# Performance work log

Measured on AMD Instinct MI355X. Metric: run time of the kernel, lower is better.

The kernel has to match this reference:

```python
import jax, jax.numpy as jnp
import numpy as np

B, T, D, H, C = 256, 512, 128, 512, 10

def setup_inputs() -> dict:
    key = jax.random.key(0)
    ks = jax.random.split(key, 16)
    def kn(k, shape):  # kaiming-normal-ish init (gain irrelevant for correctness)
        fan_in = shape[-1]
        return jax.random.normal(k, shape, dtype=jnp.float32) * (1.0 / np.sqrt(fan_in))
    return {
        "x": jax.random.randint(ks[0], (B, T), 0, 3),
        "emb": jax.random.normal(ks[1], (3, D), dtype=jnp.float32),
        "Wfx": kn(ks[2], (H, D)), "Wfh": kn(ks[3], (H, H)), "bf": jnp.zeros((H,), jnp.float32),
        "Wix": kn(ks[4], (H, D)), "Wih": kn(ks[5], (H, H)), "bi": jnp.zeros((H,), jnp.float32),
        "Wox": kn(ks[6], (H, D)), "Woh": kn(ks[7], (H, H)), "bo": jnp.zeros((H,), jnp.float32),
        "Wcx": kn(ks[8], (H, D)), "bc": jnp.zeros((H,), jnp.float32),
        "Wph": kn(ks[9], (C, H)), "bp": jnp.zeros((C,), jnp.float32),
    }

def _forward(x, emb, Wfx, Wfh, bf, Wix, Wih, bi, Wox, Woh, bo, Wcx, bc, Wph, bp):
    xe = emb[x]  # [B, T, D]
    # Precompute input-to-gate projections as one big batched matmul each.
    fx = jnp.einsum('btd,hd->bth', xe, Wfx) + bf  # [B, T, H]
    ix = jnp.einsum('btd,hd->bth', xe, Wix) + bi
    ox = jnp.einsum('btd,hd->bth', xe, Wox) + bo
    cx = jnp.einsum('btd,hd->bth', xe, Wcx) + bc
    gates = jnp.stack([fx, ix, ox, cx], axis=0).transpose(2, 1, 0, 3)  # [T, B, 4, H]

    def step(carry, g):
        c, _ = carry
        gf, gi, go, gc = g[:, 0], g[:, 1], g[:, 2], g[:, 3]  # each [B, H]
        f = jax.nn.sigmoid(gf + c @ Wfh.T)
        i = jax.nn.sigmoid(gi + c @ Wih.T)
        o = jax.nn.sigmoid(go + c @ Woh.T)
        c_new = jax.nn.sigmoid(gc) * i + c * f
        h = jnp.tanh(c_new) * o
        return (c_new, h), None

    c0 = jnp.zeros((x.shape[0], Wfh.shape[0]), jnp.float32)
    (c_fin, h_fin), _ = jax.lax.scan(step, (c0, c0), gates)
    p = h_fin @ Wph.T + bp
    return jax.nn.log_softmax(p, axis=1)

def reference(x, emb, Wfx, Wfh, bf, Wix, Wih, bi, Wox, Woh, bo, Wcx, bc, Wph, bp):
    return _forward(x, emb, Wfx, Wfh, bf, Wix, Wih, bi, Wox, Woh, bo, Wcx, bc, Wph, bp)
```

## Files before the change

### kernel.cpp

```cpp
#include <hip/hip_runtime.h>
#include <stdint.h>

#define TLEN 512
#define HDIM 512
#define DDIM 128
#define NCLS 10

typedef float f32x4 __attribute__((ext_vector_type(4)));
typedef short bf16x8 __attribute__((ext_vector_type(8)));

__device__ __forceinline__ unsigned short f2bf(float f) {
  union { float f; unsigned u; } v; v.f = f;
  return (unsigned short)((v.u + 0x7FFFu + ((v.u >> 16) & 1u)) >> 16);
}
__device__ __forceinline__ float bf2f(unsigned short h) {
  union { unsigned u; float f; } v; v.u = ((unsigned)h) << 16; return v.f;
}
__device__ __forceinline__ float sigm(float x) {
  return __builtin_amdgcn_rcpf(1.0f + __expf(-x));
}
__device__ __forceinline__ void ast16(unsigned short* p, unsigned short v) {
  __hip_atomic_store(p, v, __ATOMIC_RELAXED, __HIP_MEMORY_SCOPE_AGENT);
}
__device__ __forceinline__ void astd(unsigned* p, unsigned v) {
  __hip_atomic_store(p, v, __ATOMIC_RELAXED, __HIP_MEMORY_SCOPE_AGENT);
}

#define GLOAD_SC1(dst, addr) \
  asm volatile("global_load_dwordx4 %0, %1, off sc1" : "=&v"(dst) : "v"(addr))
#define VMWAIT() do { asm volatile("s_waitcnt vmcnt(0)" ::: "memory"); \
                      __builtin_amdgcn_sched_barrier(0); } while (0)

__global__ void k_gates(const float* __restrict__ emb,
                        const float* __restrict__ Wfx, const float* __restrict__ bf_,
                        const float* __restrict__ Wix, const float* __restrict__ bi_,
                        const float* __restrict__ Wcx, const float* __restrict__ bc_,
                        const float* __restrict__ Wox, const float* __restrict__ bo_,
                        float* __restrict__ G) {
  int tid = blockIdx.x * 256 + threadIdx.x;
  int h = tid & (HDIM - 1);
  int v = (tid >> 9) % 3;
  int g = tid / (3 * HDIM);
  const float* W; const float* bb;
  if (g == 0)      { W = Wfx; bb = bf_; }
  else if (g == 1) { W = Wix; bb = bi_; }
  else if (g == 2) { W = Wcx; bb = bc_; }
  else             { W = Wox; bb = bo_; }
  const float* e = emb + v * DDIM;
  const float* w = W + h * DDIM;
  float s = bb[h];
  #pragma unroll 8
  for (int d = 0; d < DDIM; ++d) s += e[d] * w[d];
  if (g == 2) s = sigm(s);
  G[tid] = s;
}

__global__ void k_pack_fi(const float* __restrict__ Wfh, const float* __restrict__ Wih,
                          unsigned short* __restrict__ pk) {
  int tid = blockIdx.x * 256 + threadIdx.x;
  int l  = tid & 63;
  int kt = (tid >> 6) & 15;
  int g  = (tid >> 10) & 1;
  int nt = (tid >> 11) & 3;
  int hs = (tid >> 13) & 7;
  int n  = hs * 64 + nt * 16 + (l & 15);
  int k0 = kt * 32 + (l >> 4) * 8;
  const float* src = (g ? Wih : Wfh) + n * HDIM + k0;
  unsigned short* dst = pk + (size_t)tid * 8;
  #pragma unroll
  for (int e = 0; e < 8; ++e) dst[e] = f2bf(src[e]);
}

__global__ void k_pack_o(const float* __restrict__ Woh, unsigned short* __restrict__ pk) {
  int tid = blockIdx.x * 256 + threadIdx.x;
  int l  = tid & 63;
  int kt = (tid >> 6) & 15;
  int nt = (tid >> 10) & 3;
  int hs = (tid >> 12) & 7;
  int n  = hs * 64 + nt * 16 + (l & 15);
  int k0 = kt * 32 + (l >> 4) * 8;
  const float* src = Woh + n * HDIM + k0;
  unsigned short* dst = pk + (size_t)tid * 8;
  #pragma unroll
  for (int e = 0; e < 8; ++e) dst[e] = f2bf(src[e]);
}

__global__ __launch_bounds__(256, 1)
void k_scan(const int* __restrict__ x, const float* __restrict__ G,
            const unsigned short* __restrict__ pk2,
            const unsigned short* __restrict__ pko,
            char* __restrict__ cbuf, unsigned* __restrict__ flg,
            unsigned short* __restrict__ hfin) {
  __shared__ float gts[12][68];
  __shared__ unsigned char xv[8][512];
  __shared__ uint4 lds_small[16][32];

  const int tid  = threadIdx.x;
  const int lane = tid & 63;
  const int w    = tid >> 6;
  const int hs   = blockIdx.x & 7;
  const int btg  = blockIdx.x >> 3;

  for (int jj = tid; jj < 12 * 64; jj += 256) {
    int gv = jj >> 6, c = jj & 63;
    gts[gv][c] = G[gv * HDIM + hs * 64 + c];
  }
  for (int jj = tid; jj < 8 * 512; jj += 256) {
    int r = jj >> 9, tt = jj & 511;
    xv[r][tt] = (unsigned char)x[(btg * 8 + r) * TLEN + tt];
  }
  for (int jj = tid; jj < 16 * 32; jj += 256)
    ((uint4*)lds_small)[jj] = uint4{0, 0, 0, 0};

  bf16x8 wf[16], wi[16];
  {
    const bf16x8* ws = (const bf16x8*)pk2 + (size_t)((hs * 4 + w) * 2) * (16 * 64) + lane;
    #pragma unroll
    for (int kt = 0; kt < 16; ++kt) { wf[kt] = ws[kt * 64]; wi[kt] = ws[(16 + kt) * 64]; }
  }

  bf16x8 afr[16];
  #pragma unroll
  for (int kt = 0; kt < 16; ++kt) afr[kt] = bf16x8{0,0,0,0,0,0,0,0};

  float cf[4] = {0.f, 0.f, 0.f, 0.f};
  const int rgrp = (lane >> 4) * 4;
  const int coll = lane & 15;
  const int col  = w * 16 + coll;
  const int gcol = hs * 64 + col;
  const int soff = (gcol >> 5) * 512 + (gcol & 31) * 2;
  const bool act = (lane < 32);
  const int h2   = lane >> 5;
  const int ll   = lane & 31;
  const int lrow = ll & 7, lchk = ll >> 3;
  const int kt0  = 4 * w + 2 * h2;
  const int ld0  = kt0 * 512 + lrow * 64 + lchk * 16;
  const int li   = lrow * 4 + lchk;
  const int ridx = (lane & 7) * 4 + (lane >> 4);
  const f32x4 zz = {0.f, 0.f, 0.f, 0.f};

  __syncthreads();

  for (int t = 0; t < TLEN - 1; ++t) {
    f32x4 af = zz, ai = zz;
    #pragma unroll
    for (int kt = 0; kt < 16; ++kt) {
      af = __builtin_amdgcn_mfma_f32_16x16x32_bf16(afr[kt], wf[kt], af, 0, 0, 0);
      ai = __builtin_amdgcn_mfma_f32_16x16x32_bf16(afr[kt], wi[kt], ai, 0, 0, 0);
    }
    const unsigned tg = (unsigned)(t + 1);
    const int par = (int)(tg & 1);
    char* dbase = cbuf + (size_t)(par * 32 + btg) * 8192;

    if (act) {
      #pragma unroll
      for (int r = 0; r < 4; ++r) {
        const int rr = rgrp + r;
        int vv = xv[rr][t];
        float fg = sigm(af[r] + gts[0 + vv][col]);
        float ig = sigm(ai[r] + gts[3 + vv][col]);
        float sc = gts[6 + vv][col];
        float cn = sc * ig + cf[r] * fg;
        cf[r] = cn;
        ast16((unsigned short*)(dbase + soff + rr * 64), f2bf(cn));
      }
    }
    __syncthreads();

    unsigned* fl = flg + (par * 32 + btg) * 16;
    if (tid == 0) astd(fl + hs, tg);

    const char* fb = (const char*)fl;
    uint4 f0, f1;
    do { GLOAD_SC1(f0, fb); GLOAD_SC1(f1, fb + 16); VMWAIT(); }
    while (((f0.x ^ tg) | (f0.y ^ tg) | (f0.z ^ tg) | (f0.w ^ tg) |
            (f1.x ^ tg) | (f1.y ^ tg) | (f1.z ^ tg) | (f1.w ^ tg)) != 0u);

    uint4 q0, q1;
    GLOAD_SC1(q0, dbase + ld0);
    GLOAD_SC1(q1, dbase + ld0 + 512);
    VMWAIT();
    lds_small[kt0 + 0][li] = q0;
    lds_small[kt0 + 1][li] = q1;
    __syncthreads();
    #pragma unroll
    for (int kt = 0; kt < 16; ++kt) {
      union { uint4 q; bf16x8 v; } u;
      u.q = lds_small[kt][ridx];
      afr[kt] = u.v;
    }
  }

  {
    const int t = TLEN - 1;
    f32x4 af = zz, ai = zz, ao = zz;
    #pragma unroll
    for (int kt = 0; kt < 16; ++kt) {
      af = __builtin_amdgcn_mfma_f32_16x16x32_bf16(afr[kt], wf[kt], af, 0, 0, 0);
      ai = __builtin_amdgcn_mfma_f32_16x16x32_bf16(afr[kt], wi[kt], ai, 0, 0, 0);
    }
    bf16x8 wo[16];
    const bf16x8* os = (const bf16x8*)pko + (size_t)(hs * 4 + w) * (16 * 64) + lane;
    #pragma unroll
    for (int kt = 0; kt < 16; ++kt) wo[kt] = os[kt * 64];
    #pragma unroll
    for (int kt = 0; kt < 16; ++kt)
      ao = __builtin_amdgcn_mfma_f32_16x16x32_bf16(afr[kt], wo[kt], ao, 0, 0, 0);
    if (act) {
      #pragma unroll
      for (int r = 0; r < 4; ++r) {
        const int rr = rgrp + r;
        int vv = xv[rr][t];
        float fg = sigm(af[r] + gts[0 + vv][col]);
        float ig = sigm(ai[r] + gts[3 + vv][col]);
        float sc = gts[6 + vv][col];
        float cn = sc * ig + cf[r] * fg;
        float og = sigm(ao[r] + gts[9 + vv][col]);
        float hv = tanhf(cn) * og;
        hfin[(btg * 8 + rr) * HDIM + gcol] = f2bf(hv);
      }
    }
  }
}

__global__ __launch_bounds__(64)
void k_head(const unsigned short* __restrict__ hfin, const float* __restrict__ Wph,
            const float* __restrict__ bp, float* __restrict__ out) {
  const int b = blockIdx.x;
  const int lane = threadIdx.x;
  float acc[NCLS];
  #pragma unroll
  for (int c = 0; c < NCLS; ++c) acc[c] = 0.f;
  const unsigned short* hrow = hfin + (size_t)b * HDIM;
  for (int k = lane; k < HDIM; k += 64) {
    float hv = bf2f(hrow[k]);
    #pragma unroll
    for (int c = 0; c < NCLS; ++c) acc[c] += hv * Wph[c * HDIM + k];
  }
  #pragma unroll
  for (int c = 0; c < NCLS; ++c)
    #pragma unroll
    for (int off = 32; off > 0; off >>= 1)
      acc[c] += __shfl_down(acc[c], off, 64);
  if (lane == 0) {
    float p[NCLS]; float m = -1e30f;
    #pragma unroll
    for (int c = 0; c < NCLS; ++c) { p[c] = acc[c] + bp[c]; m = fmaxf(m, p[c]); }
    float s = 0.f;
    #pragma unroll
    for (int c = 0; c < NCLS; ++c) s += __expf(p[c] - m);
    const float ls = __logf(s);
    #pragma unroll
    for (int c = 0; c < NCLS; ++c) out[b * NCLS + c] = p[c] - m - ls;
  }
}

extern "C" void kernel_launch(void* const* d_in, const int* in_sizes, int n_in,
                              void* d_out, int out_size, void* d_ws, size_t ws_size,
                              hipStream_t stream) {
  const int*   x   = (const int*)d_in[0];
  const float* emb = (const float*)d_in[1];
  const float* Wfx = (const float*)d_in[2];
  const float* Wfh = (const float*)d_in[3];
  const float* bf_ = (const float*)d_in[4];
  const float* Wix = (const float*)d_in[5];
  const float* Wih = (const float*)d_in[6];
  const float* bi_ = (const float*)d_in[7];
  const float* Wox = (const float*)d_in[8];
  const float* Woh = (const float*)d_in[9];
  const float* bo_ = (const float*)d_in[10];
  const float* Wcx = (const float*)d_in[11];
  const float* bc_ = (const float*)d_in[12];
  const float* Wph = (const float*)d_in[13];
  const float* bp_ = (const float*)d_in[14];

  char* ws = (char*)d_ws;
  float*          G    = (float*)(ws);
  unsigned*       flg  = (unsigned*)(ws + 24576);
  unsigned short* hfin = (unsigned short*)(ws + 32768);
  char*           cbuf = (char*)(ws + 524288);
  unsigned short* pk2  = (unsigned short*)(ws + 1572864);
  unsigned short* pko  = (unsigned short*)(ws + 2621440);

  hipMemsetAsync(flg, 0, 4096, stream);
  hipLaunchKernelGGL(k_gates,   dim3(24),  dim3(256), 0, stream,
                     emb, Wfx, bf_, Wix, bi_, Wcx, bc_, Wox, bo_, G);
  hipLaunchKernelGGL(k_pack_fi, dim3(256), dim3(256), 0, stream, Wfh, Wih, pk2);
  hipLaunchKernelGGL(k_pack_o,  dim3(128), dim3(256), 0, stream, Woh, pko);
  hipLaunchKernelGGL(k_scan,    dim3(256), dim3(256), 0, stream,
                     x, G, pk2, pko, cbuf, flg, hfin);
  hipLaunchKernelGGL(k_head,    dim3(256), dim3(64),  0, stream, hfin, Wph, bp_, (float*)d_out);
}
```

Measured before the change: 1.373 ms.

## Split scan into 512 blocks of 4 batch rows with single-lane flag polling

Each scan block now handles 4 batch rows instead of 8, so the grid doubles to 512 blocks and the per-group LDS, exchange buffers and flag array are resized to match. Only lane 0 of each wave spins on the cross-block flags, which cuts polling traffic. The aim is more parallelism and less per-step exchange data per block. In exchange, the 16-row MFMA tiles now carry only 4 live rows, so more MFMA work is wasted. Two blocks must share each CU, and the spin-wait protocol relies on every cooperating block being resident at once.

After: 1.375 ms. About the same (+0.1%).

```diff
diff --git a/kernel.cpp b/kernel.cpp
--- a/kernel.cpp
+++ b/kernel.cpp
@@ -92,8 +92,8 @@
             char* __restrict__ cbuf, unsigned* __restrict__ flg,
             unsigned short* __restrict__ hfin) {
   __shared__ float gts[12][68];
-  __shared__ unsigned char xv[8][512];
-  __shared__ uint4 lds_small[16][32];
+  __shared__ unsigned char xv[4][512];
+  __shared__ uint4 lds_small[16][16];
 
   const int tid  = threadIdx.x;
   const int lane = tid & 63;
@@ -105,11 +105,11 @@
     int gv = jj >> 6, c = jj & 63;
     gts[gv][c] = G[gv * HDIM + hs * 64 + c];
   }
-  for (int jj = tid; jj < 8 * 512; jj += 256) {
+  for (int jj = tid; jj < 4 * 512; jj += 256) {
     int r = jj >> 9, tt = jj & 511;
-    xv[r][tt] = (unsigned char)x[(btg * 8 + r) * TLEN + tt];
-  }
-  for (int jj = tid; jj < 16 * 32; jj += 256)
+    xv[r][tt] = (unsigned char)x[(btg * 4 + r) * TLEN + tt];
+  }
+  for (int jj = tid; jj < 16 * 16; jj += 256)
     ((uint4*)lds_small)[jj] = uint4{0, 0, 0, 0};
 
   bf16x8 wf[16], wi[16];
@@ -124,19 +124,15 @@
   for (int kt = 0; kt < 16; ++kt) afr[kt] = bf16x8{0,0,0,0,0,0,0,0};
 
   float cf[4] = {0.f, 0.f, 0.f, 0.f};
-  const int rgrp = (lane >> 4) * 4;
   const int coll = lane & 15;
   const int col  = w * 16 + coll;
   const int gcol = hs * 64 + col;
-  const int soff = (gcol >> 5) * 512 + (gcol & 31) * 2;
-  const bool act = (lane < 32);
-  const int h2   = lane >> 5;
-  const int ll   = lane & 31;
-  const int lrow = ll & 7, lchk = ll >> 3;
-  const int kt0  = 4 * w + 2 * h2;
-  const int ld0  = kt0 * 512 + lrow * 64 + lchk * 16;
-  const int li   = lrow * 4 + lchk;
-  const int ridx = (lane & 7) * 4 + (lane >> 4);
+  const int soff = (gcol >> 5) * 256 + (gcol & 31) * 2;
+  const bool act = (lane < 16);
+  const int ldkt = 4 * w + (lane >> 4);
+  const int ldof = ldkt * 256 + ((lane >> 2) & 3) * 64 + (lane & 3) * 16;
+  const int sidx = (lane & 3) * 4 + ((lane >> 2) & 3);
+  const int ridx = (lane >> 4) * 4 + (lane & 3);
   const f32x4 zz = {0.f, 0.f, 0.f, 0.f};
 
   __syncthreads();
@@ -150,43 +146,41 @@
     }
     const unsigned tg = (unsigned)(t + 1);
     const int par = (int)(tg & 1);
-    char* dbase = cbuf + (size_t)(par * 32 + btg) * 8192;
+    char* dbase = cbuf + (size_t)(par * 64 + btg) * 4096;
 
     if (act) {
       #pragma unroll
       for (int r = 0; r < 4; ++r) {
-        const int rr = rgrp + r;
-        int vv = xv[rr][t];
+        int vv = xv[r][t];
         float fg = sigm(af[r] + gts[0 + vv][col]);
         float ig = sigm(ai[r] + gts[3 + vv][col]);
         float sc = gts[6 + vv][col];
         float cn = sc * ig + cf[r] * fg;
         cf[r] = cn;
-        ast16((unsigned short*)(dbase + soff + rr * 64), f2bf(cn));
+        ast16((unsigned short*)(dbase + soff + r * 64), f2bf(cn));
       }
     }
     __syncthreads();
 
-    unsigned* fl = flg + (par * 32 + btg) * 16;
+    unsigned* fl = flg + (par * 64 + btg) * 16;
     if (tid == 0) astd(fl + hs, tg);
 
-    const char* fb = (const char*)fl;
-    uint4 f0, f1;
-    do { GLOAD_SC1(f0, fb); GLOAD_SC1(f1, fb + 16); VMWAIT(); }
-    while (((f0.x ^ tg) | (f0.y ^ tg) | (f0.z ^ tg) | (f0.w ^ tg) |
-            (f1.x ^ tg) | (f1.y ^ tg) | (f1.z ^ tg) | (f1.w ^ tg)) != 0u);
-
-    uint4 q0, q1;
-    GLOAD_SC1(q0, dbase + ld0);
-    GLOAD_SC1(q1, dbase + ld0 + 512);
+    if (lane == 0) {
+      uint4 f0, f1;
+      do { GLOAD_SC1(f0, (const char*)fl); GLOAD_SC1(f1, (const char*)fl + 16); VMWAIT(); }
+      while (((f0.x ^ tg) | (f0.y ^ tg) | (f0.z ^ tg) | (f0.w ^ tg) |
+              (f1.x ^ tg) | (f1.y ^ tg) | (f1.z ^ tg) | (f1.w ^ tg)) != 0u);
+    }
+
+    uint4 q;
+    GLOAD_SC1(q, dbase + ldof);
     VMWAIT();
-    lds_small[kt0 + 0][li] = q0;
-    lds_small[kt0 + 1][li] = q1;
+    lds_small[ldkt][sidx] = q;
     __syncthreads();
     #pragma unroll
     for (int kt = 0; kt < 16; ++kt) {
-      union { uint4 q; bf16x8 v; } u;
-      u.q = lds_small[kt][ridx];
+      union { uint4 qq; bf16x8 v; } u;
+      u.qq = lds_small[kt][ridx];
       afr[kt] = u.v;
     }
   }
@@ -209,15 +203,14 @@
     if (act) {
       #pragma unroll
       for (int r = 0; r < 4; ++r) {
-        const int rr = rgrp + r;
-        int vv = xv[rr][t];
+        int vv = xv[r][t];
         float fg = sigm(af[r] + gts[0 + vv][col]);
         float ig = sigm(ai[r] + gts[3 + vv][col]);
         float sc = gts[6 + vv][col];
         float cn = sc * ig + cf[r] * fg;
         float og = sigm(ao[r] + gts[9 + vv][col]);
         float hv = tanhf(cn) * og;
-        hfin[(btg * 8 + rr) * HDIM + gcol] = f2bf(hv);
+        hfin[(btg * 4 + r) * HDIM + gcol] = f2bf(hv);
       }
     }
   }
@@ -282,12 +275,12 @@
   unsigned short* pk2  = (unsigned short*)(ws + 1572864);
   unsigned short* pko  = (unsigned short*)(ws + 2621440);
 
-  hipMemsetAsync(flg, 0, 4096, stream);
+  hipMemsetAsync(flg, 0, 8192, stream);
   hipLaunchKernelGGL(k_gates,   dim3(24),  dim3(256), 0, stream,
                      emb, Wfx, bf_, Wix, bi_, Wcx, bc_, Wox, bo_, G);
   hipLaunchKernelGGL(k_pack_fi, dim3(256), dim3(256), 0, stream, Wfh, Wih, pk2);
   hipLaunchKernelGGL(k_pack_o,  dim3(128), dim3(256), 0, stream, Woh, pko);
-  hipLaunchKernelGGL(k_scan,    dim3(256), dim3(256), 0, stream,
+  hipLaunchKernelGGL(k_scan,    dim3(512), dim3(256), 0, stream,
                      x, G, pk2, pko, cbuf, flg, hfin);
   hipLaunchKernelGGL(k_head,    dim3(256), dim3(64),  0, stream, hfin, Wph, bp_, (float*)d_out);
 }
```
